# Optimization experiments

Hardware: AMD Instinct MI355X
Metric: run time of the kernel (lower is better)

Reference implementation:

```python
import jax, jax.numpy as jnp
import numpy as np

B, S, D, H, E = 2, 1024, 1024, 4096, 8


def _xavier(key, shape):
    # matches torch.nn.init.xavier_uniform_ on a 3D tensor: fan_in/out from last two dims
    fan_in, fan_out = shape[-2], shape[-1]
    limit = float(np.sqrt(6.0 / (fan_in + fan_out)))
    return jax.random.uniform(key, shape, jnp.float32, -limit, limit)


def setup_inputs() -> dict:
    key = jax.random.key(0)
    ks = jax.random.split(key, 4)
    x = jax.random.normal(ks[0], (B, S, D), jnp.float32)
    router_w = jax.random.normal(ks[1], (D, E), jnp.float32) * (1.0 / np.sqrt(D))
    router_b = jnp.zeros((E,), jnp.float32)
    fc1_weight = _xavier(ks[2], (E, D, H))
    fc1_bias = jnp.zeros((E, H), jnp.float32)
    fc2_weight = _xavier(ks[3], (E, H, D))
    fc2_bias = jnp.zeros((E, D), jnp.float32)
    return {
        "x": x,
        "router_w": router_w,
        "router_b": router_b,
        "fc1_weight": fc1_weight,
        "fc1_bias": fc1_bias,
        "fc2_weight": fc2_weight,
        "fc2_bias": fc2_bias,
    }


def reference(x, router_w, router_b, fc1_weight, fc1_bias, fc2_weight, fc2_bias):
    b, s, d = x.shape
    x_flat = x.reshape(-1, d)                                  # [T, D]
    logits = x_flat @ router_w + router_b                       # [T, E]
    probs = jax.nn.softmax(logits, axis=-1)                     # [T, E]
    # per-expert FC1 + exact GELU (torch nn.GELU default is erf-based)
    h = jnp.einsum('td,edh->teh', x_flat, fc1_weight) + fc1_bias  # [T, E, H]
    h = jax.nn.gelu(h, approximate=False)
    expert_out = jnp.einsum('teh,ehd->ted', h, fc2_weight) + fc2_bias  # [T, E, D]
    out_flat = jnp.einsum('te,ted->td', probs, expert_out)      # [T, D]
    y = out_flat.reshape(b, s, d)
    router_probs = probs.reshape(b, s, -1)
    return y, router_probs
```

## Files before the change

kernel.cpp:

```cpp
#include <hip/hip_runtime.h>
#include <math.h>


typedef float f32x4 __attribute__((ext_vector_type(4)));
typedef __bf16 bf16x8 __attribute__((ext_vector_type(8)));

#define GLL16(gp, lp)                                                          \
  __builtin_amdgcn_global_load_lds(                                            \
      (const __attribute__((address_space(1))) void*)(gp),                     \
      (__attribute__((address_space(3))) void*)(lp), 16, 0, 0)

__device__ __forceinline__ float gelu_f(float h) {
  float x = h * 0.70710678118654752f;
  float ax = fabsf(x);
  float t = __builtin_amdgcn_rcpf(fmaf(0.3275911f, ax, 1.0f));
  float p = fmaf(1.061405429f, t, -1.453152027f);
  p = fmaf(p, t, 1.421413741f);
  p = fmaf(p, t, -0.284496736f);
  p = fmaf(p, t, 0.254829592f);
  float e = __expf(-x * x);
  float erfv = fmaf(-p * t, e, 1.0f);
  erfv = copysignf(erfv, x);
  return 0.5f * h * (1.0f + erfv);
}

__global__ void pre_kernel(const float* __restrict__ x,
                           const float* __restrict__ rw,
                           const float* __restrict__ rb,
                           const float* __restrict__ b2,
                           float* __restrict__ PT,
                           float* __restrict__ probs_out,
                           __bf16* __restrict__ xb,
                           float* __restrict__ y)
{
  __shared__ float ps[4][8];
  const int tid = threadIdx.x;
  const int g = tid >> 6, l = tid & 63;
  const int t = blockIdx.x * 4 + g;
  const int d0 = l * 16;
  const float* xr = x + (size_t)t * 1024 + d0;

  f32x4 xv[4];
#pragma unroll
  for (int i = 0; i < 4; ++i) xv[i] = *(const f32x4*)(xr + i * 4);

  {
    bf16x8 o0, o1;
#pragma unroll
    for (int j = 0; j < 8; ++j) {
      o0[j] = (__bf16)xv[j >> 2][j & 3];
      o1[j] = (__bf16)xv[2 + (j >> 2)][j & 3];
    }
    *(bf16x8*)(xb + (size_t)t * 1024 + d0) = o0;
    *(bf16x8*)(xb + (size_t)t * 1024 + d0 + 8) = o1;
  }

  float a[8];
#pragma unroll
  for (int e = 0; e < 8; ++e) a[e] = 0.f;
#pragma unroll
  for (int i = 0; i < 16; ++i) {
    float xs = xv[i >> 2][i & 3];
    const float* wr = rw + (size_t)(d0 + i) * 8;
    f32x4 w0 = *(const f32x4*)(wr);
    f32x4 w1 = *(const f32x4*)(wr + 4);
#pragma unroll
    for (int e = 0; e < 4; ++e) a[e] = fmaf(xs, w0[e], a[e]);
#pragma unroll
    for (int e = 0; e < 4; ++e) a[4 + e] = fmaf(xs, w1[e], a[4 + e]);
  }
#pragma unroll
  for (int off = 32; off > 0; off >>= 1) {
#pragma unroll
    for (int e = 0; e < 8; ++e) a[e] += __shfl_down(a[e], off);
  }
  if (l == 0) {
#pragma unroll
    for (int e = 0; e < 8; ++e) a[e] += rb[e];
    float m = a[0];
#pragma unroll
    for (int e = 1; e < 8; ++e) m = fmaxf(m, a[e]);
    float s = 0.f;
#pragma unroll
    for (int e = 0; e < 8; ++e) { a[e] = __expf(a[e] - m); s += a[e]; }
    float inv = 1.f / s;
#pragma unroll
    for (int e = 0; e < 8; ++e) {
      float p = a[e] * inv;
      PT[(size_t)e * 2048 + t] = p;
      probs_out[t * 8 + e] = p;
      ps[g][e] = p;
    }
  }
  __syncthreads();

  f32x4 acc[4];
#pragma unroll
  for (int i = 0; i < 4; ++i) acc[i] = {0.f, 0.f, 0.f, 0.f};
#pragma unroll
  for (int e = 0; e < 8; ++e) {
    float p = ps[g][e];
#pragma unroll
    for (int i = 0; i < 4; ++i) {
      f32x4 b = *(const f32x4*)(b2 + (size_t)e * 1024 + d0 + i * 4);
#pragma unroll
      for (int c = 0; c < 4; ++c) acc[i][c] = fmaf(p, b[c], acc[i][c]);
    }
  }
#pragma unroll
  for (int i = 0; i < 4; ++i)
    *(f32x4*)(y + (size_t)t * 1024 + d0 + i * 4) = acc[i];
}

__global__ void router_kernel(const float* __restrict__ x,
                              const float* __restrict__ rw,
                              const float* __restrict__ rb,
                              float* __restrict__ probs_out)
{
  int gid = blockIdx.x * blockDim.x + threadIdx.x;
  int t = gid >> 6;
  int l = gid & 63;
  const float* xr = x + (size_t)t * 1024;
  float a[8];
#pragma unroll
  for (int e = 0; e < 8; ++e) a[e] = 0.f;
  for (int d = l; d < 1024; d += 64) {
    float xv = xr[d];
    f32x4 w0 = *(const f32x4*)(rw + d * 8);
    f32x4 w1 = *(const f32x4*)(rw + d * 8 + 4);
#pragma unroll
    for (int e = 0; e < 4; ++e) a[e] += xv * w0[e];
#pragma unroll
    for (int e = 0; e < 4; ++e) a[4 + e] += xv * w1[e];
  }
#pragma unroll
  for (int off = 32; off > 0; off >>= 1) {
#pragma unroll
    for (int e = 0; e < 8; ++e) a[e] += __shfl_down(a[e], off);
  }
  if (l == 0) {
#pragma unroll
    for (int e = 0; e < 8; ++e) a[e] += rb[e];
    float m = a[0];
#pragma unroll
    for (int e = 1; e < 8; ++e) m = fmaxf(m, a[e]);
    float s = 0.f;
#pragma unroll
    for (int e = 0; e < 8; ++e) { a[e] = __expf(a[e] - m); s += a[e]; }
    float inv = 1.f / s;
#pragma unroll
    for (int e = 0; e < 8; ++e) probs_out[t * 8 + e] = a[e] * inv;
  }
}

__device__ __forceinline__ void transconv_body(const float* __restrict__ src,
                                               __bf16* __restrict__ dst,
                                               int R, int C, size_t dstLd,
                                               size_t zOff)
{
  __shared__ __bf16 tile[64][257];
  size_t bs = (size_t)blockIdx.z * (size_t)R * (size_t)C;
  size_t dzo = (size_t)blockIdx.z * zOff;
  int r0 = blockIdx.x * 64, c0 = blockIdx.y * 256;
  const int l15 = (threadIdx.x & 15) * 4;
  const int rq = threadIdx.x >> 4;
#pragma unroll
  for (int i = 0; i < 4; ++i) {
    const int row = rq + 16 * i;
    const float* sr = src + bs + (size_t)(r0 + row) * C + c0 + l15;
#pragma unroll
    for (int q = 0; q < 4; ++q) {
      f32x4 v = *(const f32x4*)(sr + q * 64);
#pragma unroll
      for (int j = 0; j < 4; ++j)
        tile[row][q * 64 + l15 + j] = (__bf16)v[j];
    }
  }
  __syncthreads();
  const int cb = threadIdx.x >> 3;
  const int orr = (threadIdx.x & 7) * 8;
#pragma unroll
  for (int g = 0; g < 8; ++g) {
    const int c = cb + 32 * g;
    bf16x8 o;
#pragma unroll
    for (int j = 0; j < 8; ++j) o[j] = tile[orr + j][c];
    *(bf16x8*)(dst + (size_t)(c0 + c) * dstLd + dzo + r0 + orr) = o;
  }
}

__global__ void transconv1_kernel(const float* __restrict__ src,
                                  __bf16* __restrict__ dst,
                                  int R, int C, size_t dstLd, size_t zOff)
{ transconv_body(src, dst, R, C, dstLd, zOff); }

__global__ void transconv2_kernel(const float* __restrict__ src,
                                  __bf16* __restrict__ dst,
                                  int R, int C, size_t dstLd, size_t zOff)
{ transconv_body(src, dst, R, C, dstLd, zOff); }

__device__ __forceinline__ void mfma_loop256(
    const char* Ab, const char* Bb, size_t ldaB, size_t ldbB, int K,
    char* lds, f32x4 acc[8][4])
{
  const int tid = threadIdx.x;
  const int w = tid >> 6, l = tid & 63;
  const int wm = w >> 2, wn = w & 3;
  const int m16 = l & 15, q = l >> 4;
  const int swz = m16 & 7;
  const int aBase = wm * 16384 + m16 * 128;
  const int bBase = 32768 + (wn >> 1) * 16384 + ((wn & 1) * 64 + m16) * 128;
  const int srcCh = ((l & 7) ^ ((l >> 3) & 7)) << 4;
  const size_t gA0 = (size_t)(w * 16 + (l >> 3)) * ldaB + srcCh;
  const size_t gB0 = (size_t)(w * 16 + (l >> 3)) * ldbB + srcCh;
  const int dstW = w * 2048;
  const int NT = K >> 6;

  bf16x8 af[4][2], bv[4][2];

#define STG_A(h, tau)                                                          \
  {                                                                            \
    char* d = lds + (((tau) & 1) * 65536) + (h) * 16384 + dstW;                \
    const char* g = Ab + gA0 + (size_t)((h) * 128) * ldaB + (size_t)(tau) * 128;\
    GLL16(g, d);                                                               \
    GLL16(g + 8 * ldaB, d + 1024);                                             \
  }
#define STG_B(h, tau)                                                          \
  {                                                                            \
    char* d = lds + (((tau) & 1) * 65536) + 32768 + (h) * 16384 + dstW;        \
    const char* g = Bb + gB0 + (size_t)((h) * 128) * ldbB + (size_t)(tau) * 128;\
    GLL16(g, d);                                                               \
    GLL16(g + 8 * ldbB, d + 1024);                                             \
  }
#define RD_A(lo, p)                                                            \
  _Pragma("unroll") for (int mi = 0; mi < 4; ++mi)                             \
  _Pragma("unroll") for (int ks = 0; ks < 2; ++ks)                             \
    af[mi][ks] = *(const bf16x8*)(lds + (p) * 65536 + aBase +                  \
        ((lo) * 4 + mi) * 2048 + (((ks * 4 + q) ^ swz) << 4));
#define RD_B(no, p)                                                            \
  _Pragma("unroll") for (int nj = 0; nj < 2; ++nj)                             \
  _Pragma("unroll") for (int ks = 0; ks < 2; ++ks)                             \
    bv[(no) * 2 + nj][ks] = *(const bf16x8*)(lds + (p) * 65536 + bBase +       \
        ((no) * 2 + nj) * 2048 + (((ks * 4 + q) ^ swz) << 4));
#define MM(lo, no)                                                             \
  _Pragma("unroll") for (int mi = 0; mi < 4; ++mi)                             \
  _Pragma("unroll") for (int nj = 0; nj < 2; ++nj)                             \
  _Pragma("unroll") for (int ks = 0; ks < 2; ++ks)                             \
    acc[(lo) * 4 + mi][(no) * 2 + nj] =                                        \
        __builtin_amdgcn_mfma_f32_16x16x32_bf16(                               \
            af[mi][ks], bv[(no) * 2 + nj][ks],                                 \
            acc[(lo) * 4 + mi][(no) * 2 + nj], 0, 0, 0);
#define MMP(lo)                                                                \
  __builtin_amdgcn_s_setprio(1);                                               \
  MM(lo, 0); MM(lo, 1);                                                        \
  __builtin_amdgcn_s_setprio(0);
#define BARR __builtin_amdgcn_s_barrier()
#define VMW(n) asm volatile("s_waitcnt vmcnt(" #n ")" ::: "memory")

  STG_A(0, 0); STG_A(1, 0); STG_B(0, 0); STG_B(1, 0);
  STG_B(0, 1); STG_B(1, 1);
  VMW(4);
  BARR;

  int t = 0;
  for (; t < NT - 2; ++t) {
    const int p = t & 1;
    RD_B(0, p); RD_B(1, p); RD_A(0, p);
    STG_A(0, t + 1); STG_A(1, t + 1);
    MMP(0);
    BARR;
    STG_B(0, t + 2); STG_B(1, t + 2);
    RD_A(1, p);
    MMP(1);
    VMW(4);
    BARR;
  }
  {
    const int p = t & 1;
    RD_B(0, p); RD_B(1, p); RD_A(0, p);
    STG_A(0, t + 1); STG_A(1, t + 1);
    MMP(0);
    BARR;
    RD_A(1, p);
    MMP(1);
    VMW(0);
    BARR;
    ++t;
  }
  {
    const int p = t & 1;
    RD_B(0, p); RD_B(1, p); RD_A(0, p);
    MMP(0);
    RD_A(1, p);
    MMP(1);
  }
#undef STG_A
#undef STG_B
#undef RD_A
#undef RD_B
#undef MM
#undef MMP
#undef BARR
#undef VMW
}

__device__ __forceinline__ int xcd_swz(int id, int nwg) {
  return ((nwg & 7) == 0) ? ((id & 7) * (nwg >> 3) + (id >> 3)) : id;
}

__global__ __launch_bounds__(512, 2) void gemm1_kernel(
    const __bf16* __restrict__ X, const __bf16* __restrict__ W1T,
    const float* __restrict__ b1, const float* __restrict__ PT,
    __bf16* __restrict__ Hs, int hs_ld, int e_off, size_t b_zstride)
{
  __shared__ __align__(16) char lds[131072];
  const int nwg = gridDim.x * gridDim.y * gridDim.z;
  const int id = blockIdx.x + gridDim.x * (blockIdx.y + gridDim.y * blockIdx.z);
  const int wg = xcd_swz(id, nwg);
  const int bm = wg & 7;
  const int bn = (wg >> 3) % gridDim.y;
  const int z = wg / (gridDim.y << 3);
  const int e = z + e_off;

  f32x4 acc[8][4];
  const f32x4 z4 = {0.f, 0.f, 0.f, 0.f};
#pragma unroll
  for (int i = 0; i < 8; ++i)
#pragma unroll
    for (int j = 0; j < 4; ++j) acc[i][j] = z4;

  const char* A = (const char*)(X + (size_t)bm * 256 * 1024);
  const char* B = (const char*)(W1T + (size_t)z * b_zstride +
                                (size_t)bn * 256 * 1024);
  mfma_loop256(A, B, 2048, 2048, 1024, lds, acc);

  const int tid = threadIdx.x, w = tid >> 6, l = tid & 63;
  const int wm = w >> 2, wn = w & 3, q = l >> 4, m16 = l & 15;
  const int row0 = bm * 256 + wm * 128 + q * 4;
  const int colE = bn * 256 + wn * 64 + m16;
  const int zcol = (hs_ld == 4096) ? 0 : z * 4096;
  float b1v[4];
#pragma unroll
  for (int nj = 0; nj < 4; ++nj)
    b1v[nj] = b1[(size_t)e * 4096 + colE + nj * 16];
#pragma unroll
  for (int mi = 0; mi < 8; ++mi) {
    float pv[4];
#pragma unroll
    for (int r = 0; r < 4; ++r)
      pv[r] = PT[(size_t)e * 2048 + row0 + mi * 16 + r];
#pragma unroll
    for (int nj = 0; nj < 4; ++nj)
#pragma unroll
      for (int r = 0; r < 4; ++r) {
        float h = acc[mi][nj][r] + b1v[nj];
        float o = gelu_f(h) * pv[r];
        Hs[(size_t)(row0 + mi * 16 + r) * hs_ld + zcol + colE + nj * 16] =
            (__bf16)o;
      }
  }
}

__global__ __launch_bounds__(512, 2) void gemm2_kernel(
    const __bf16* __restrict__ Hs, const __bf16* __restrict__ W2T,
    float* __restrict__ y, int lda, int ldb, int kz, int Kb)
{
  __shared__ __align__(16) char lds[131072];
  const int nwg = gridDim.x * gridDim.y * gridDim.z;
  const int id = blockIdx.x + gridDim.x * (blockIdx.y + gridDim.y * blockIdx.z);
  const int wg = xcd_swz(id, nwg);
  const int bm = wg & 7;
  const int bn = (wg >> 3) % gridDim.y;
  const int z = wg / (gridDim.y << 3);

  f32x4 acc[8][4];
  const f32x4 z4 = {0.f, 0.f, 0.f, 0.f};
#pragma unroll
  for (int i = 0; i < 8; ++i)
#pragma unroll
    for (int j = 0; j < 4; ++j) acc[i][j] = z4;

  const char* A = (const char*)(Hs + (size_t)bm * 256 * lda + (size_t)z * kz);
  const char* B = (const char*)(W2T + (size_t)bn * 256 * ldb + (size_t)z * kz);
  mfma_loop256(A, B, (size_t)lda * 2, (size_t)ldb * 2, Kb, lds, acc);

  const int tid = threadIdx.x, w = tid >> 6, l = tid & 63;
  const int wm = w >> 2, wn = w & 3, q = l >> 4, m16 = l & 15;
  const int row0 = bm * 256 + wm * 128 + q * 4;
  const int col0 = bn * 256 + wn * 64 + m16;
#pragma unroll
  for (int mi = 0; mi < 8; ++mi)
#pragma unroll
    for (int nj = 0; nj < 4; ++nj)
#pragma unroll
      for (int r = 0; r < 4; ++r)
        unsafeAtomicAdd(
            y + (size_t)(row0 + mi * 16 + r) * 1024 + col0 + nj * 16,
            acc[mi][nj][r]);
}

__global__ __launch_bounds__(256) void fused_naive_kernel(
    const float* __restrict__ x, const float* __restrict__ w1,
    const float* __restrict__ b1, const float* __restrict__ w2,
    const float* __restrict__ b2, const float* __restrict__ probs,
    float* __restrict__ y)
{
  __shared__ float xs[8][1024];
  __shared__ float gs[8][64];
  __shared__ float ps[8];
  const int tid = threadIdx.x;
  const int t0 = blockIdx.x * 8;
  const size_t DH = (size_t)1024 * 4096;
  const int tt = tid >> 5;
  const int d0 = (tid & 31) * 32;
  float acc[32];
#pragma unroll
  for (int i = 0; i < 32; ++i) acc[i] = 0.f;
  {
    const f32x4* xsrc = (const f32x4*)(x + (size_t)t0 * 1024);
    f32x4* xdst = (f32x4*)&xs[0][0];
    for (int i = tid; i < 2048; i += 256) xdst[i] = xsrc[i];
  }
  const int wv = tid >> 6;
  const int hl = tid & 63;
  for (int e = 0; e < 8; ++e) {
    if (tid < 8) ps[tid] = probs[(size_t)(t0 + tid) * 8 + e];
    __syncthreads();
    for (int hc = 0; hc < 4096; hc += 64) {
      float a0 = 0.f, a1 = 0.f;
      const float* w1p = w1 + (size_t)e * DH + hc + hl;
      for (int d = 0; d < 1024; ++d) {
        float wvv = w1p[(size_t)d * 4096];
        a0 += xs[wv * 2 + 0][d] * wvv;
        a1 += xs[wv * 2 + 1][d] * wvv;
      }
      __syncthreads();
      gs[wv * 2 + 0][hl] =
          ps[wv * 2 + 0] * gelu_f(a0 + b1[(size_t)e * 4096 + hc + hl]);
      gs[wv * 2 + 1][hl] =
          ps[wv * 2 + 1] * gelu_f(a1 + b1[(size_t)e * 4096 + hc + hl]);
      __syncthreads();
      const float* w2p = w2 + (size_t)e * DH + (size_t)hc * 1024 + d0;
      for (int hh = 0; hh < 64; ++hh) {
        float g = gs[tt][hh];
#pragma unroll
        for (int jb = 0; jb < 8; ++jb) {
          f32x4 w4 = *(const f32x4*)(w2p + (size_t)hh * 1024 + jb * 4);
#pragma unroll
          for (int j2 = 0; j2 < 4; ++j2) acc[jb * 4 + j2] += g * w4[j2];
        }
      }
    }
#pragma unroll
    for (int j = 0; j < 32; ++j)
      acc[j] += ps[tt] * b2[(size_t)e * 1024 + d0 + j];
    __syncthreads();
  }
  float* yp = y + (size_t)(t0 + tt) * 1024 + d0;
#pragma unroll
  for (int jb = 0; jb < 8; ++jb) {
    f32x4 o = {acc[jb * 4], acc[jb * 4 + 1], acc[jb * 4 + 2], acc[jb * 4 + 3]};
    *(f32x4*)(yp + jb * 4) = o;
  }
}

extern "C" void kernel_launch(void* const* d_in, const int* in_sizes, int n_in,
                              void* d_out, int out_size, void* d_ws,
                              size_t ws_size, hipStream_t stream)
{
  const float* x  = (const float*)d_in[0];
  const float* rw = (const float*)d_in[1];
  const float* rb = (const float*)d_in[2];
  const float* w1 = (const float*)d_in[3];
  const float* b1 = (const float*)d_in[4];
  const float* w2 = (const float*)d_in[5];
  const float* b2 = (const float*)d_in[6];
  float* y = (float*)d_out;
  float* probs_out = y + (size_t)2048 * 1024;

  const size_t DH = (size_t)1024 * 4096;
  const size_t BASE = (64 << 10) + (size_t)2048 * 1024 * 2;
  const size_t TA = BASE + 8 * DH * 2 + (size_t)2048 * 32768 * 2;
  const size_t TB = BASE + DH * 2 + (size_t)2048 * 4096 * 2;

  char* ws = (char*)d_ws;
  float* PT = (float*)ws;
  __bf16* xb = (__bf16*)(ws + (64 << 10));
  __bf16* WT = (__bf16*)(ws + BASE);

  if (ws_size >= TA) {
    pre_kernel<<<512, 256, 0, stream>>>(x, rw, rb, b2, PT, probs_out, xb, y);
    __bf16* Hs = WT + 8 * DH;
    transconv1_kernel<<<dim3(16, 16, 8), 256, 0, stream>>>(
        w1, WT, 1024, 4096, 1024, DH);
    gemm1_kernel<<<dim3(8, 16, 8), 512, 0, stream>>>(xb, WT, b1, PT, Hs,
                                                     32768, 0, DH);
    transconv2_kernel<<<dim3(64, 4, 8), 256, 0, stream>>>(
        w2, WT, 4096, 1024, 32768, 4096);
    gemm2_kernel<<<dim3(8, 4, 8), 512, 0, stream>>>(Hs, WT, y, 32768,
                                                    32768, 4096, 4096);
  } else if (ws_size >= TB) {
    pre_kernel<<<512, 256, 0, stream>>>(x, rw, rb, b2, PT, probs_out, xb, y);
    __bf16* HsE = WT + DH;
    for (int e = 0; e < 8; ++e) {
      transconv1_kernel<<<dim3(16, 16, 1), 256, 0, stream>>>(
          w1 + (size_t)e * DH, WT, 1024, 4096, 1024, 0);
      gemm1_kernel<<<dim3(8, 16, 1), 512, 0, stream>>>(xb, WT, b1, PT, HsE,
                                                       4096, e, 0);
      transconv2_kernel<<<dim3(64, 4, 1), 256, 0, stream>>>(
          w2 + (size_t)e * DH, WT, 4096, 1024, 4096, 0);
      gemm2_kernel<<<dim3(8, 4, 4), 512, 0, stream>>>(HsE, WT, y, 4096,
                                                      4096, 1024, 1024);
    }
  } else {
    router_kernel<<<512, 256, 0, stream>>>(x, rw, rb, probs_out);
    fused_naive_kernel<<<256, 256, 0, stream>>>(x, w1, b1, w2, b2, probs_out,
                                                y);
  }
}
```

Before: 609.8 us.

## Fuse weight transpose-convert into GEMM B-operand loading, drop transconv kernels

Removes the separate transpose+bf16 conversion kernels for fc1/fc2 weights and instead has each GEMM workgroup gather fp32 weights directly from global memory, convert them to bf16 in registers, and write them into LDS in the expected layout. This avoids writing and re-reading a bf16 copy of all expert weights (and two extra launches). In exchange, B-operand loads become strided scalar fp32 global reads with one-tile lookahead and a full vmcnt/lgkmcnt drain each iteration, weakening the software pipeline. Each B tile is also re-read as fp32 by every M-block (8 per expert), which raises global traffic.

```diff
diff --git a/kernel.cpp b/kernel.cpp
--- a/kernel.cpp
+++ b/kernel.cpp
@@ -153,55 +153,9 @@
   }
 }
 
-__device__ __forceinline__ void transconv_body(const float* __restrict__ src,
-                                               __bf16* __restrict__ dst,
-                                               int R, int C, size_t dstLd,
-                                               size_t zOff)
-{
-  __shared__ __bf16 tile[64][257];
-  size_t bs = (size_t)blockIdx.z * (size_t)R * (size_t)C;
-  size_t dzo = (size_t)blockIdx.z * zOff;
-  int r0 = blockIdx.x * 64, c0 = blockIdx.y * 256;
-  const int l15 = (threadIdx.x & 15) * 4;
-  const int rq = threadIdx.x >> 4;
-#pragma unroll
-  for (int i = 0; i < 4; ++i) {
-    const int row = rq + 16 * i;
-    const float* sr = src + bs + (size_t)(r0 + row) * C + c0 + l15;
-#pragma unroll
-    for (int q = 0; q < 4; ++q) {
-      f32x4 v = *(const f32x4*)(sr + q * 64);
-#pragma unroll
-      for (int j = 0; j < 4; ++j)
-        tile[row][q * 64 + l15 + j] = (__bf16)v[j];
-    }
-  }
-  __syncthreads();
-  const int cb = threadIdx.x >> 3;
-  const int orr = (threadIdx.x & 7) * 8;
-#pragma unroll
-  for (int g = 0; g < 8; ++g) {
-    const int c = cb + 32 * g;
-    bf16x8 o;
-#pragma unroll
-    for (int j = 0; j < 8; ++j) o[j] = tile[orr + j][c];
-    *(bf16x8*)(dst + (size_t)(c0 + c) * dstLd + dzo + r0 + orr) = o;
-  }
-}
-
-__global__ void transconv1_kernel(const float* __restrict__ src,
-                                  __bf16* __restrict__ dst,
-                                  int R, int C, size_t dstLd, size_t zOff)
-{ transconv_body(src, dst, R, C, dstLd, zOff); }
-
-__global__ void transconv2_kernel(const float* __restrict__ src,
-                                  __bf16* __restrict__ dst,
-                                  int R, int C, size_t dstLd, size_t zOff)
-{ transconv_body(src, dst, R, C, dstLd, zOff); }
-
 __device__ __forceinline__ void mfma_loop256(
-    const char* Ab, const char* Bb, size_t ldaB, size_t ldbB, int K,
-    char* lds, f32x4 acc[8][4])
+    const char* Ab, size_t ldaB, const float* __restrict__ Bf, int ldN,
+    int K, char* lds, f32x4 acc[8][4])
 {
   const int tid = threadIdx.x;
   const int w = tid >> 6, l = tid & 63;
@@ -212,11 +166,13 @@
   const int bBase = 32768 + (wn >> 1) * 16384 + ((wn & 1) * 64 + m16) * 128;
   const int srcCh = ((l & 7) ^ ((l >> 3) & 7)) << 4;
   const size_t gA0 = (size_t)(w * 16 + (l >> 3)) * ldaB + srcCh;
-  const size_t gB0 = (size_t)(w * 16 + (l >> 3)) * ldbB + srcCh;
   const int dstW = w * 2048;
+  const int kOff = ((l & 7) ^ (l >> 3)) * 8;
+  const int nB = w * 16 + (l >> 3);
   const int NT = K >> 6;
 
   bf16x8 af[4][2], bv[4][2];
+  float gq[4][8];
 
 #define STG_A(h, tau)                                                          \
   {                                                                            \
@@ -225,12 +181,21 @@
     GLL16(g, d);                                                               \
     GLL16(g + 8 * ldaB, d + 1024);                                             \
   }
-#define STG_B(h, tau)                                                          \
-  {                                                                            \
-    char* d = lds + (((tau) & 1) * 65536) + 32768 + (h) * 16384 + dstW;        \
-    const char* g = Bb + gB0 + (size_t)((h) * 128) * ldbB + (size_t)(tau) * 128;\
-    GLL16(g, d);                                                               \
-    GLL16(g + 8 * ldbB, d + 1024);                                             \
+#define GATH(tau)                                                              \
+  _Pragma("unroll") for (int hh = 0; hh < 2; ++hh)                             \
+  _Pragma("unroll") for (int uu = 0; uu < 2; ++uu)                             \
+  _Pragma("unroll") for (int j = 0; j < 8; ++j)                                \
+    gq[hh * 2 + uu][j] =                                                       \
+        Bf[(size_t)((tau) * 64 + kOff + j) * (size_t)ldN +                     \
+           (nB + hh * 128 + uu * 8)];
+#define WRB(tau)                                                               \
+  _Pragma("unroll") for (int hh = 0; hh < 2; ++hh)                             \
+  _Pragma("unroll") for (int uu = 0; uu < 2; ++uu) {                           \
+    bf16x8 vv;                                                                 \
+    _Pragma("unroll") for (int j = 0; j < 8; ++j)                              \
+      vv[j] = (__bf16)gq[hh * 2 + uu][j];                                      \
+    *(bf16x8*)(lds + (((tau) & 1) * 65536) + 32768 + hh * 16384 + dstW +       \
+               uu * 1024 + l * 16) = vv;                                       \
   }
 #define RD_A(lo, p)                                                            \
   _Pragma("unroll") for (int mi = 0; mi < 4; ++mi)                             \
@@ -255,37 +220,26 @@
   MM(lo, 0); MM(lo, 1);                                                        \
   __builtin_amdgcn_s_setprio(0);
 #define BARR __builtin_amdgcn_s_barrier()
-#define VMW(n) asm volatile("s_waitcnt vmcnt(" #n ")" ::: "memory")
-
-  STG_A(0, 0); STG_A(1, 0); STG_B(0, 0); STG_B(1, 0);
-  STG_B(0, 1); STG_B(1, 1);
-  VMW(4);
+#define DRAIN asm volatile("s_waitcnt vmcnt(0) lgkmcnt(0)" ::: "memory")
+
+  GATH(0);
+  STG_A(0, 0); STG_A(1, 0);
+  WRB(0);
+  DRAIN;
   BARR;
 
   int t = 0;
-  for (; t < NT - 2; ++t) {
+  for (; t < NT - 1; ++t) {
     const int p = t & 1;
     RD_B(0, p); RD_B(1, p); RD_A(0, p);
+    GATH(t + 1);
     STG_A(0, t + 1); STG_A(1, t + 1);
     MMP(0);
+    RD_A(1, p);
+    WRB(t + 1);
+    MMP(1);
+    DRAIN;
     BARR;
-    STG_B(0, t + 2); STG_B(1, t + 2);
-    RD_A(1, p);
-    MMP(1);
-    VMW(4);
-    BARR;
-  }
-  {
-    const int p = t & 1;
-    RD_B(0, p); RD_B(1, p); RD_A(0, p);
-    STG_A(0, t + 1); STG_A(1, t + 1);
-    MMP(0);
-    BARR;
-    RD_A(1, p);
-    MMP(1);
-    VMW(0);
-    BARR;
-    ++t;
   }
   {
     const int p = t & 1;
@@ -295,13 +249,14 @@
     MMP(1);
   }
 #undef STG_A
-#undef STG_B
+#undef GATH
+#undef WRB
 #undef RD_A
 #undef RD_B
 #undef MM
 #undef MMP
 #undef BARR
-#undef VMW
+#undef DRAIN
 }
 
 __device__ __forceinline__ int xcd_swz(int id, int nwg) {
@@ -309,7 +264,7 @@
 }
 
 __global__ __launch_bounds__(512, 2) void gemm1_kernel(
-    const __bf16* __restrict__ X, const __bf16* __restrict__ W1T,
+    const __bf16* __restrict__ X, const float* __restrict__ W1,
     const float* __restrict__ b1, const float* __restrict__ PT,
     __bf16* __restrict__ Hs, int hs_ld, int e_off, size_t b_zstride)
 {
@@ -330,9 +285,8 @@
     for (int j = 0; j < 4; ++j) acc[i][j] = z4;
 
   const char* A = (const char*)(X + (size_t)bm * 256 * 1024);
-  const char* B = (const char*)(W1T + (size_t)z * b_zstride +
-                                (size_t)bn * 256 * 1024);
-  mfma_loop256(A, B, 2048, 2048, 1024, lds, acc);
+  const float* Bf = W1 + (size_t)z * b_zstride + (size_t)bn * 256;
+  mfma_loop256(A, 2048, Bf, 4096, 1024, lds, acc);
 
   const int tid = threadIdx.x, w = tid >> 6, l = tid & 63;
   const int wm = w >> 2, wn = w & 3, q = l >> 4, m16 = l & 15;
@@ -362,8 +316,8 @@
 }
 
 __global__ __launch_bounds__(512, 2) void gemm2_kernel(
-    const __bf16* __restrict__ Hs, const __bf16* __restrict__ W2T,
-    float* __restrict__ y, int lda, int ldb, int kz, int Kb)
+    const __bf16* __restrict__ Hs, const float* __restrict__ W2,
+    float* __restrict__ y, int lda, int kz, size_t b_zstride, int Kb)
 {
   __shared__ __align__(16) char lds[131072];
   const int nwg = gridDim.x * gridDim.y * gridDim.z;
@@ -381,8 +335,8 @@
     for (int j = 0; j < 4; ++j) acc[i][j] = z4;
 
   const char* A = (const char*)(Hs + (size_t)bm * 256 * lda + (size_t)z * kz);
-  const char* B = (const char*)(W2T + (size_t)bn * 256 * ldb + (size_t)z * kz);
-  mfma_loop256(A, B, (size_t)lda * 2, (size_t)ldb * 2, Kb, lds, acc);
+  const float* Bf = W2 + (size_t)z * b_zstride + (size_t)bn * 256;
+  mfma_loop256(A, (size_t)lda * 2, Bf, 1024, Kb, lds, acc);
 
   const int tid = threadIdx.x, w = tid >> 6, l = tid & 63;
   const int wm = w >> 2, wn = w & 3, q = l >> 4, m16 = l & 15;
@@ -480,37 +434,28 @@
 
   const size_t DH = (size_t)1024 * 4096;
   const size_t BASE = (64 << 10) + (size_t)2048 * 1024 * 2;
-  const size_t TA = BASE + 8 * DH * 2 + (size_t)2048 * 32768 * 2;
-  const size_t TB = BASE + DH * 2 + (size_t)2048 * 4096 * 2;
+  const size_t TA = BASE + (size_t)2048 * 32768 * 2;
+  const size_t TB = BASE + (size_t)2048 * 4096 * 2;
 
   char* ws = (char*)d_ws;
   float* PT = (float*)ws;
   __bf16* xb = (__bf16*)(ws + (64 << 10));
-  __bf16* WT = (__bf16*)(ws + BASE);
+  __bf16* Hs = (__bf16*)(ws + BASE);
 
   if (ws_size >= TA) {
     pre_kernel<<<512, 256, 0, stream>>>(x, rw, rb, b2, PT, probs_out, xb, y);
-    __bf16* Hs = WT + 8 * DH;
-    transconv1_kernel<<<dim3(16, 16, 8), 256, 0, stream>>>(
-        w1, WT, 1024, 4096, 1024, DH);
-    gemm1_kernel<<<dim3(8, 16, 8), 512, 0, stream>>>(xb, WT, b1, PT, Hs,
+    gemm1_kernel<<<dim3(8, 16, 8), 512, 0, stream>>>(xb, w1, b1, PT, Hs,
                                                      32768, 0, DH);
-    transconv2_kernel<<<dim3(64, 4, 8), 256, 0, stream>>>(
-        w2, WT, 4096, 1024, 32768, 4096);
-    gemm2_kernel<<<dim3(8, 4, 8), 512, 0, stream>>>(Hs, WT, y, 32768,
-                                                    32768, 4096, 4096);
+    gemm2_kernel<<<dim3(8, 4, 8), 512, 0, stream>>>(Hs, w2, y, 32768,
+                                                    4096, DH, 4096);
   } else if (ws_size >= TB) {
     pre_kernel<<<512, 256, 0, stream>>>(x, rw, rb, b2, PT, probs_out, xb, y);
-    __bf16* HsE = WT + DH;
     for (int e = 0; e < 8; ++e) {
-      transconv1_kernel<<<dim3(16, 16, 1), 256, 0, stream>>>(
-          w1 + (size_t)e * DH, WT, 1024, 4096, 1024, 0);
-      gemm1_kernel<<<dim3(8, 16, 1), 512, 0, stream>>>(xb, WT, b1, PT, HsE,
-                                                       4096, e, 0);
-      transconv2_kernel<<<dim3(64, 4, 1), 256, 0, stream>>>(
-          w2 + (size_t)e * DH, WT, 4096, 1024, 4096, 0);
-      gemm2_kernel<<<dim3(8, 4, 4), 512, 0, stream>>>(HsE, WT, y, 4096,
-                                                      4096, 1024, 1024);
+      gemm1_kernel<<<dim3(8, 16, 1), 512, 0, stream>>>(
+          xb, w1 + (size_t)e * DH, b1, PT, Hs, 4096, e, 0);
+      gemm2_kernel<<<dim3(8, 4, 4), 512, 0, stream>>>(
+          Hs, w2 + (size_t)e * DH, y, 4096, 1024,
+          (size_t)1024 * 1024, 1024);
     }
   } else {
     router_kernel<<<512, 256, 0, stream>>>(x, rw, rb, probs_out);
```

New measurement: 1.356 ms. 2.22x slower.
